# Kernel tuning notes

Hardware: AMD Instinct MI355X
Metric: run time of the kernel (lower is better)

## Reference

```python
import jax, jax.numpy as jnp
import numpy as np

N_NODES = 200000
N_ETYPES = 4
N_EDGES = 500000
D_IN = 128
D_OUT = 128


def setup_inputs() -> dict:
    key = jax.random.key(0)
    ks = jax.random.split(key, 7)
    scale = 1.0 / np.sqrt(D_IN)
    x = jax.random.normal(ks[0], (N_NODES, D_IN), dtype=jnp.float32)
    W = jax.random.normal(ks[1], (N_ETYPES, D_IN, D_OUT), dtype=jnp.float32) * scale
    b = jax.random.normal(ks[2], (N_ETYPES, D_OUT), dtype=jnp.float32) * 0.01
    W_self = jax.random.normal(ks[3], (D_IN, D_OUT), dtype=jnp.float32) * scale
    b_self = jax.random.normal(ks[4], (D_OUT,), dtype=jnp.float32) * 0.01
    src = jax.random.randint(ks[5], (N_ETYPES, N_EDGES), 0, N_NODES, dtype=jnp.int32)
    dst = jax.random.randint(ks[6], (N_ETYPES, N_EDGES), 0, N_NODES, dtype=jnp.int32)
    return {"x": x, "W": W, "b": b, "W_self": W_self, "b_self": b_self,
            "src": src, "dst": dst}


def _etype_mean_agg(Wx_e, src_e, dst_e, n_nodes):
    # gather transformed src features along edges, mean-reduce per dst node
    m = Wx_e[src_e]  # [E, d_out]
    s = jax.ops.segment_sum(m, dst_e, num_segments=n_nodes)  # [N, d_out]
    cnt = jax.ops.segment_sum(jnp.ones((src_e.shape[0],), dtype=Wx_e.dtype),
                              dst_e, num_segments=n_nodes)  # [N]
    # nodes with no in-edges of this etype contribute 0 (DGL leaves h unset -> 0)
    return jnp.where(cnt[:, None] > 0, s / jnp.maximum(cnt[:, None], 1.0), 0.0)


def reference(x, W, b, W_self, b_self, src, dst):
    n_nodes = x.shape[0]
    # per-etype linear transform of all node features: [T, N, d_out]
    Wx = jnp.einsum('nd,tdf->tnf', x, W) + b[:, None, :]
    # per-etype gather + segment mean, then sum across etypes ('sum' cross-reducer)
    h = jax.vmap(_etype_mean_agg, in_axes=(0, 0, 0, None))(Wx, src, dst, n_nodes)
    h = h.sum(axis=0)  # [N, d_out]
    self_msg = x @ W_self + b_self
    return self_msg + h
```

## Files before the change

kernel.cpp:

```cpp
#include <hip/hip_runtime.h>
#include <hip/hip_bf16.h>


namespace {

constexpr int N  = 200000;
constexpr int T  = 4;
constexpr int E  = 500000;
constexpr int D  = 128;
constexpr int NT = 64;
constexpr int AS = 136;

constexpr int CNT_B = (T * E + 255) / 256;
constexpr int PX_B  = (N * D / 8) / 256;
constexpr int PW_B  = (5 * D * D / 8 + 255) / 256;

typedef __bf16 bf16x8 __attribute__((ext_vector_type(8)));
typedef float  f32x4  __attribute__((ext_vector_type(4)));

__global__ void k_zero(int* __restrict__ p, int n) {
  int i = blockIdx.x * 256 + threadIdx.x;
  if (i < n) p[i] = 0;
}

template <bool XB>
__global__ void k_prep(const int* __restrict__ dst, int* __restrict__ cnt,
                       int* __restrict__ rank, const float* __restrict__ x,
                       __bf16* __restrict__ xb, const float* __restrict__ W,
                       const float* __restrict__ Wself, __bf16* __restrict__ wt) {
  const int bid = blockIdx.x;
  const int tid = threadIdx.x;
  if (bid < CNT_B) {
    int i = bid * 256 + tid;
    if (i < T * E) {
      int t = i / E;
      rank[i] = atomicAdd(&cnt[t * N + dst[i]], 1);
    }
  } else if (XB && bid < CNT_B + PX_B) {
    int i = (bid - CNT_B) * 256 + tid;
    if (i < N * D / 8) {
      const float4* xs = (const float4*)(x + i * 8);
      float4 a = xs[0], c = xs[1];
      bf16x8 v;
      v[0] = (__bf16)a.x; v[1] = (__bf16)a.y; v[2] = (__bf16)a.z; v[3] = (__bf16)a.w;
      v[4] = (__bf16)c.x; v[5] = (__bf16)c.y; v[6] = (__bf16)c.z; v[7] = (__bf16)c.w;
      *(bf16x8*)(xb + i * 8) = v;
    }
  } else {
    int i = (bid - CNT_B - (XB ? PX_B : 0)) * 256 + tid;
    if (i < 5 * D * D / 8) {
      int base = i * 8;
      int p = base >> 14, rem = base & 16383;
      int n = rem >> 7, k0 = rem & 127;
      const float* Wsrc = (p < 4) ? (W + (size_t)p * D * D) : Wself;
      bf16x8 v;
#pragma unroll
      for (int j = 0; j < 8; ++j) v[j] = (__bf16)Wsrc[(k0 + j) * D + n];
      *(bf16x8*)(wt + base) = v;
    }
  }
}

__global__ void k_offsets(const int* __restrict__ cnt, int* __restrict__ offs,
                          int* __restrict__ cursor) {
  __shared__ int s[256];
  __shared__ int base;
  int tid = threadIdx.x;
  int i = blockIdx.x * 256 + tid;
  int c = (i < T * N) ? cnt[i] : 0;
  s[tid] = c;
  __syncthreads();
  for (int d = 1; d < 256; d <<= 1) {
    int v = (tid >= d) ? s[tid - d] : 0;
    __syncthreads();
    s[tid] += v;
    __syncthreads();
  }
  if (tid == 255) base = atomicAdd(cursor, s[255]);
  __syncthreads();
  if (i < T * N) offs[i] = base + s[tid] - c;
}

__global__ void k_scatter(const int* __restrict__ src, const int* __restrict__ dst,
                          const int* __restrict__ offs, const int* __restrict__ rank,
                          int* __restrict__ eid) {
  int i = blockIdx.x * 256 + threadIdx.x;
  if (i >= T * E) return;
  int t = i / E;
  int pos = offs[t * N + dst[i]] + rank[i];
  eid[pos] = src[i];
}

template <bool XB>
__global__ __launch_bounds__(256, 3) void k_fused(
    const float* __restrict__ x, const __bf16* __restrict__ xb,
    const __bf16* __restrict__ wt, const float* __restrict__ b,
    const float* __restrict__ bself, const int* __restrict__ cnt,
    const int* __restrict__ offs, const int* __restrict__ eid,
    float* __restrict__ out) {
  __shared__ __align__(16) __bf16 a_s[NT * AS];
  __shared__ __align__(16) __bf16 w_s[D * AS];

  const int tid  = threadIdx.x;
  const int nb   = blockIdx.x * NT;
  const int wv   = tid >> 6;
  const int lane = tid & 63;
  const int quad = lane >> 4;
  const int l16  = lane & 15;
  const int ln   = tid >> 2;
  const int q    = tid & 3;

  f32x4 acc[8];
#pragma unroll
  for (int ct = 0; ct < 8; ++ct) acc[ct] = (f32x4){0.f, 0.f, 0.f, 0.f};

  for (int pass = 0; pass < 5; ++pass) {
    const bool self = (pass == 4);

    {
      const __bf16* wsrc = wt + pass * D * D;
#pragma unroll
      for (int c = 0; c < 8; ++c) {
        int idx  = c * 256 + tid;
        int row  = idx >> 4;
        int col8 = (idx & 15) * 8;
        *(bf16x8*)(w_s + row * AS + col8) = *(const bf16x8*)(wsrc + row * D + col8);
      }
    }

    if (!(XB && self)) {
      float r[32];
#pragma unroll
      for (int i = 0; i < 32; ++i) r[i] = 0.f;
      const int node = nb + ln;
      if (self) {
        const float4* xr = (const float4*)(x + node * D + q * 32);
#pragma unroll
        for (int i = 0; i < 8; ++i) {
          float4 v = xr[i];
          r[4 * i] = v.x; r[4 * i + 1] = v.y; r[4 * i + 2] = v.z; r[4 * i + 3] = v.w;
        }
      } else {
        const int base = offs[pass * N + node];
        const int deg  = cnt[pass * N + node];
        int nxt = (deg > 0) ? eid[base] : 0;
        for (int e = 0; e < deg; ++e) {
          const int sidx = nxt;
          nxt = eid[base + e + 1];
          if (XB) {
            const bf16x8* xr = (const bf16x8*)(xb + sidx * D + q * 32);
            bf16x8 v0 = xr[0], v1 = xr[1], v2 = xr[2], v3 = xr[3];
#pragma unroll
            for (int j = 0; j < 8; ++j) {
              r[j]      += (float)v0[j];
              r[8 + j]  += (float)v1[j];
              r[16 + j] += (float)v2[j];
              r[24 + j] += (float)v3[j];
            }
          } else {
            const float4* xr = (const float4*)(x + sidx * D + q * 32);
#pragma unroll
            for (int i = 0; i < 8; ++i) {
              float4 v = xr[i];
              r[4 * i] += v.x; r[4 * i + 1] += v.y;
              r[4 * i + 2] += v.z; r[4 * i + 3] += v.w;
            }
          }
        }
        const float inv = (deg > 0) ? (1.0f / (float)deg) : 0.0f;
#pragma unroll
        for (int i = 0; i < 32; ++i) r[i] *= inv;
      }
      __bf16* arow = a_s + ln * AS + q * 32;
#pragma unroll
      for (int g = 0; g < 4; ++g) {
        bf16x8 v;
#pragma unroll
        for (int j = 0; j < 8; ++j) v[j] = (__bf16)r[8 * g + j];
        *(bf16x8*)(arow + g * 8) = v;
      }
    }
    __syncthreads();

#pragma unroll
    for (int ks = 0; ks < 4; ++ks) {
      bf16x8 af;
      if (XB && self) {
        af = *(const bf16x8*)(xb + (nb + 16 * wv + l16) * D + ks * 32 + quad * 8);
      } else {
        af = *(const bf16x8*)(a_s + (16 * wv + l16) * AS + ks * 32 + quad * 8);
      }
#pragma unroll
      for (int ct = 0; ct < 8; ++ct) {
        bf16x8 bfr = *(const bf16x8*)(w_s + (16 * ct + l16) * AS + ks * 32 + quad * 8);
        acc[ct] = __builtin_amdgcn_mfma_f32_16x16x32_bf16(af, bfr, acc[ct], 0, 0, 0);
      }
    }

    {
      const float* bt = self ? bself : (b + pass * D);
      bool rowon[4];
#pragma unroll
      for (int r = 0; r < 4; ++r) {
        rowon[r] = self ? true : (cnt[pass * N + nb + 16 * wv + quad * 4 + r] > 0);
      }
#pragma unroll
      for (int ct = 0; ct < 8; ++ct) {
        float bv = bt[16 * ct + l16];
#pragma unroll
        for (int r = 0; r < 4; ++r)
          if (rowon[r]) acc[ct][r] += bv;
      }
    }
    if (pass < 4) __syncthreads();
  }

#pragma unroll
  for (int ct = 0; ct < 8; ++ct) {
#pragma unroll
    for (int r = 0; r < 4; ++r) {
      out[(nb + 16 * wv + quad * 4 + r) * D + 16 * ct + l16] = acc[ct][r];
    }
  }
}

}

extern "C" void kernel_launch(void* const* d_in, const int* in_sizes, int n_in,
                              void* d_out, int out_size, void* d_ws, size_t ws_size,
                              hipStream_t stream) {
  const float* x     = (const float*)d_in[0];
  const float* W     = (const float*)d_in[1];
  const float* b     = (const float*)d_in[2];
  const float* Wself = (const float*)d_in[3];
  const float* bself = (const float*)d_in[4];
  const int*   src   = (const int*)d_in[5];
  const int*   dst   = (const int*)d_in[6];
  float* out = (float*)d_out;

  int* cnt    = (int*)d_ws;
  int* cursor = cnt + T * N;
  int* offs   = cursor + 4;
  int* eid    = offs + T * N;
  int* rank   = eid + T * E;
  __bf16* wt  = (__bf16*)(rank + T * E);
  __bf16* xb  = wt + 5 * D * D;

  const size_t need_xb =
      (size_t)(T * N + 4 + T * N + T * E + T * E) * 4 + (size_t)5 * D * D * 2 +
      (size_t)N * D * 2;
  const bool use_xb = ws_size >= need_xb;

  k_zero<<<(T * N + 4 + 255) / 256, 256, 0, stream>>>(cnt, T * N + 4);
  if (use_xb) {
    k_prep<true><<<CNT_B + PX_B + PW_B, 256, 0, stream>>>(dst, cnt, rank, x, xb,
                                                          W, Wself, wt);
  } else {
    k_prep<false><<<CNT_B + PW_B, 256, 0, stream>>>(dst, cnt, rank, x, xb, W,
                                                    Wself, wt);
  }
  k_offsets<<<(T * N + 255) / 256, 256, 0, stream>>>(cnt, offs, cursor);
  k_scatter<<<(T * E + 255) / 256, 256, 0, stream>>>(src, dst, offs, rank, eid);
  if (use_xb) {
    k_fused<true><<<N / NT, 256, 0, stream>>>(x, xb, wt, b, bself, cnt, offs,
                                              eid, out);
  } else {
    k_fused<false><<<N / NT, 256, 0, stream>>>(x, xb, wt, b, bself, cnt, offs,
                                               eid, out);
  }
}
```

Baseline: 544.9 us.

## Gather edges block-wide with LDS float atomics instead of per-node serial loops

The aggregation is now edge-parallel across the whole 64-node tile: each group of four threads takes one edge from the block's contiguous CSR range and atomically adds the source row into a swizzled fp32 LDS accumulator. The destination's local index is packed into the low bits of eid. The point is to remove the load imbalance and serial dependency of per-node degree loops. W fragments are now read straight from global/L2 rather than staged in LDS, which shrinks LDS use and lets occupancy be raised to 4. The cost is many LDS atomics per edge, with contention when edges share a destination.

New measurement: 1.790 ms. 3.29x slower.

```diff
diff --git a/kernel.cpp b/kernel.cpp
--- a/kernel.cpp
+++ b/kernel.cpp
@@ -9,7 +9,6 @@
 constexpr int E  = 500000;
 constexpr int D  = 128;
 constexpr int NT = 64;
-constexpr int AS = 136;
 
 constexpr int CNT_B = (T * E + 255) / 256;
 constexpr int PX_B  = (N * D / 8) / 256;
@@ -87,19 +86,19 @@
   int i = blockIdx.x * 256 + threadIdx.x;
   if (i >= T * E) return;
   int t = i / E;
-  int pos = offs[t * N + dst[i]] + rank[i];
-  eid[pos] = src[i];
+  int d = dst[i];
+  int pos = offs[t * N + d] + rank[i];
+  eid[pos] = (src[i] << 6) | (d & 63);
 }
 
 template <bool XB>
-__global__ __launch_bounds__(256, 3) void k_fused(
+__global__ __launch_bounds__(256, 4) void k_fused(
     const float* __restrict__ x, const __bf16* __restrict__ xb,
     const __bf16* __restrict__ wt, const float* __restrict__ b,
     const float* __restrict__ bself, const int* __restrict__ cnt,
     const int* __restrict__ offs, const int* __restrict__ eid,
     float* __restrict__ out) {
-  __shared__ __align__(16) __bf16 a_s[NT * AS];
-  __shared__ __align__(16) __bf16 w_s[D * AS];
+  __shared__ __align__(16) float accf[NT * D];
 
   const int tid  = threadIdx.x;
   const int nb   = blockIdx.x * NT;
@@ -107,7 +106,7 @@
   const int lane = tid & 63;
   const int quad = lane >> 4;
   const int l16  = lane & 15;
-  const int ln   = tid >> 2;
+  const int grp  = tid >> 2;
   const int q    = tid & 3;
 
   f32x4 acc[8];
@@ -117,82 +116,160 @@
   for (int pass = 0; pass < 5; ++pass) {
     const bool self = (pass == 4);
 
-    {
-      const __bf16* wsrc = wt + pass * D * D;
-#pragma unroll
-      for (int c = 0; c < 8; ++c) {
-        int idx  = c * 256 + tid;
-        int row  = idx >> 4;
-        int col8 = (idx & 15) * 8;
-        *(bf16x8*)(w_s + row * AS + col8) = *(const bf16x8*)(wsrc + row * D + col8);
-      }
-    }
-
-    if (!(XB && self)) {
-      float r[32];
-#pragma unroll
-      for (int i = 0; i < 32; ++i) r[i] = 0.f;
-      const int node = nb + ln;
+    if (!self) {
+      if (pass) __syncthreads();
+      {
+        f32x4* z4 = (f32x4*)accf;
+        const f32x4 z = {0.f, 0.f, 0.f, 0.f};
+#pragma unroll
+        for (int k2 = 0; k2 < 8; ++k2) z4[k2 * 256 + tid] = z;
+      }
+      __syncthreads();
+
+      const int b0    = pass * N + nb;
+      const int base  = offs[b0];
+      const int nedge = offs[b0 + NT - 1] + cnt[b0 + NT - 1] - base;
+
+      for (int it = 0; it < nedge; it += 128) {
+        const int i0 = it + grp;
+        const int i1 = i0 + 64;
+        const int u0 = (i0 < nedge) ? eid[base + i0] : 0;
+        const int u1 = (i1 < nedge) ? eid[base + i1] : 0;
+        if (XB) {
+          const char* p0 = (const char*)(xb + (size_t)(u0 >> 6) * D + q * 8);
+          const char* p1 = (const char*)(xb + (size_t)(u1 >> 6) * D + q * 8);
+          int4 m0[4], m1[4];
+#pragma unroll
+          for (int l = 0; l < 4; ++l) m0[l] = *(const int4*)(p0 + l * 64);
+#pragma unroll
+          for (int l = 0; l < 4; ++l) m1[l] = *(const int4*)(p1 + l * 64);
+          if (i0 < nedge) {
+            const int dl  = u0 & 63;
+            const int key = dl & 31;
+            float* rowp = accf + dl * 128;
+#pragma unroll
+            for (int l = 0; l < 4; ++l) {
+              const unsigned uu[4] = {(unsigned)m0[l].x, (unsigned)m0[l].y,
+                                      (unsigned)m0[l].z, (unsigned)m0[l].w};
+#pragma unroll
+              for (int p2 = 0; p2 < 4; ++p2) {
+                const int c0 = l * 32 + q * 8 + 2 * p2;
+                atomicAdd(rowp + (c0 ^ key), __uint_as_float(uu[p2] << 16));
+                atomicAdd(rowp + ((c0 + 1) ^ key),
+                          __uint_as_float(uu[p2] & 0xffff0000u));
+              }
+            }
+          }
+          if (i1 < nedge) {
+            const int dl  = u1 & 63;
+            const int key = dl & 31;
+            float* rowp = accf + dl * 128;
+#pragma unroll
+            for (int l = 0; l < 4; ++l) {
+              const unsigned uu[4] = {(unsigned)m1[l].x, (unsigned)m1[l].y,
+                                      (unsigned)m1[l].z, (unsigned)m1[l].w};
+#pragma unroll
+              for (int p2 = 0; p2 < 4; ++p2) {
+                const int c0 = l * 32 + q * 8 + 2 * p2;
+                atomicAdd(rowp + (c0 ^ key), __uint_as_float(uu[p2] << 16));
+                atomicAdd(rowp + ((c0 + 1) ^ key),
+                          __uint_as_float(uu[p2] & 0xffff0000u));
+              }
+            }
+          }
+        } else {
+          const float* p0 = x + (size_t)(u0 >> 6) * D + q * 8;
+          const float* p1 = x + (size_t)(u1 >> 6) * D + q * 8;
+          f32x4 a0[8], a1[8];
+#pragma unroll
+          for (int l = 0; l < 4; ++l) {
+            a0[2 * l]     = *(const f32x4*)(p0 + l * 32);
+            a0[2 * l + 1] = *(const f32x4*)(p0 + l * 32 + 4);
+          }
+#pragma unroll
+          for (int l = 0; l < 4; ++l) {
+            a1[2 * l]     = *(const f32x4*)(p1 + l * 32);
+            a1[2 * l + 1] = *(const f32x4*)(p1 + l * 32 + 4);
+          }
+          if (i0 < nedge) {
+            const int dl  = u0 & 63;
+            const int key = dl & 31;
+            float* rowp = accf + dl * 128;
+#pragma unroll
+            for (int l = 0; l < 4; ++l)
+#pragma unroll
+              for (int w = 0; w < 4; ++w) {
+                const int c0 = l * 32 + q * 8 + w;
+                atomicAdd(rowp + (c0 ^ key), a0[2 * l][w]);
+                atomicAdd(rowp + ((c0 + 4) ^ key), a0[2 * l + 1][w]);
+              }
+          }
+          if (i1 < nedge) {
+            const int dl  = u1 & 63;
+            const int key = dl & 31;
+            float* rowp = accf + dl * 128;
+#pragma unroll
+            for (int l = 0; l < 4; ++l)
+#pragma unroll
+              for (int w = 0; w < 4; ++w) {
+                const int c0 = l * 32 + q * 8 + w;
+                atomicAdd(rowp + (c0 ^ key), a1[2 * l][w]);
+                atomicAdd(rowp + ((c0 + 4) ^ key), a1[2 * l + 1][w]);
+              }
+          }
+        }
+      }
+      __syncthreads();
+
+      {
+        const int ln   = grp;
+        const int keyr = ln & 31;
+        const int deg  = cnt[b0 + ln];
+        const float inv = (deg > 0) ? (1.0f / (float)deg) : 0.f;
+        const float* rp = accf + ln * 128;
+        float rv[32];
+#pragma unroll
+        for (int idx = 0; idx < 32; ++idx) rv[idx] = rp[(q * 32 + idx) ^ keyr];
+        __syncthreads();
+        __bf16* ab = (__bf16*)accf;
+#pragma unroll
+        for (int g = 0; g < 4; ++g) {
+          bf16x8 vv;
+#pragma unroll
+          for (int j2 = 0; j2 < 8; ++j2) vv[j2] = (__bf16)(rv[g * 8 + j2] * inv);
+          *(bf16x8*)(ab + ln * 128 + ((q * 32 + g * 8) ^ ((ln & 7) << 3))) = vv;
+        }
+      }
+      __syncthreads();
+    }
+
+#pragma unroll
+    for (int ks = 0; ks < 4; ++ks) {
+      bf16x8 af;
       if (self) {
-        const float4* xr = (const float4*)(x + node * D + q * 32);
-#pragma unroll
-        for (int i = 0; i < 8; ++i) {
-          float4 v = xr[i];
-          r[4 * i] = v.x; r[4 * i + 1] = v.y; r[4 * i + 2] = v.z; r[4 * i + 3] = v.w;
+        if (XB) {
+          af = *(const bf16x8*)(xb + (size_t)(nb + 16 * wv + l16) * D + ks * 32 +
+                                quad * 8);
+        } else {
+          const float* xr =
+              x + (size_t)(nb + 16 * wv + l16) * D + ks * 32 + quad * 8;
+          f32x4 v0 = *(const f32x4*)xr, v1 = *(const f32x4*)(xr + 4);
+#pragma unroll
+          for (int j2 = 0; j2 < 4; ++j2) {
+            af[j2] = (__bf16)v0[j2];
+            af[4 + j2] = (__bf16)v1[j2];
+          }
         }
       } else {
-        const int base = offs[pass * N + node];
-        const int deg  = cnt[pass * N + node];
-        int nxt = (deg > 0) ? eid[base] : 0;
-        for (int e = 0; e < deg; ++e) {
-          const int sidx = nxt;
-          nxt = eid[base + e + 1];
-          if (XB) {
-            const bf16x8* xr = (const bf16x8*)(xb + sidx * D + q * 32);
-            bf16x8 v0 = xr[0], v1 = xr[1], v2 = xr[2], v3 = xr[3];
-#pragma unroll
-            for (int j = 0; j < 8; ++j) {
-              r[j]      += (float)v0[j];
-              r[8 + j]  += (float)v1[j];
-              r[16 + j] += (float)v2[j];
-              r[24 + j] += (float)v3[j];
-            }
-          } else {
-            const float4* xr = (const float4*)(x + sidx * D + q * 32);
-#pragma unroll
-            for (int i = 0; i < 8; ++i) {
-              float4 v = xr[i];
-              r[4 * i] += v.x; r[4 * i + 1] += v.y;
-              r[4 * i + 2] += v.z; r[4 * i + 3] += v.w;
-            }
-          }
-        }
-        const float inv = (deg > 0) ? (1.0f / (float)deg) : 0.0f;
-#pragma unroll
-        for (int i = 0; i < 32; ++i) r[i] *= inv;
-      }
-      __bf16* arow = a_s + ln * AS + q * 32;
-#pragma unroll
-      for (int g = 0; g < 4; ++g) {
-        bf16x8 v;
-#pragma unroll
-        for (int j = 0; j < 8; ++j) v[j] = (__bf16)r[8 * g + j];
-        *(bf16x8*)(arow + g * 8) = v;
-      }
-    }
-    __syncthreads();
-
-#pragma unroll
-    for (int ks = 0; ks < 4; ++ks) {
-      bf16x8 af;
-      if (XB && self) {
-        af = *(const bf16x8*)(xb + (nb + 16 * wv + l16) * D + ks * 32 + quad * 8);
-      } else {
-        af = *(const bf16x8*)(a_s + (16 * wv + l16) * AS + ks * 32 + quad * 8);
-      }
+        const __bf16* ab = (const __bf16*)accf;
+        const int row = 16 * wv + l16;
+        af = *(const bf16x8*)(ab + row * 128 +
+                              ((ks * 32 + quad * 8) ^ ((row & 7) << 3)));
+      }
+      const __bf16* wp = wt + pass * D * D + ks * 32 + quad * 8;
 #pragma unroll
       for (int ct = 0; ct < 8; ++ct) {
-        bf16x8 bfr = *(const bf16x8*)(w_s + (16 * ct + l16) * AS + ks * 32 + quad * 8);
+        bf16x8 bfr = *(const bf16x8*)(wp + (16 * ct + l16) * D);
         acc[ct] = __builtin_amdgcn_mfma_f32_16x16x32_bf16(af, bfr, acc[ct], 0, 0, 0);
       }
     }
@@ -206,20 +283,19 @@
       }
 #pragma unroll
       for (int ct = 0; ct < 8; ++ct) {
-        float bv = bt[16 * ct + l16];
+        const float bv = bt[16 * ct + l16];
 #pragma unroll
         for (int r = 0; r < 4; ++r)
           if (rowon[r]) acc[ct][r] += bv;
       }
     }
-    if (pass < 4) __syncthreads();
   }
 
 #pragma unroll
   for (int ct = 0; ct < 8; ++ct) {
 #pragma unroll
     for (int r = 0; r < 4; ++r) {
-      out[(nb + 16 * wv + quad * 4 + r) * D + 16 * ct + l16] = acc[ct][r];
+      out[(size_t)(nb + 16 * wv + quad * 4 + r) * D + 16 * ct + l16] = acc[ct][r];
     }
   }
 }
```
